# Performance work log

Measured on AMD Instinct MI355X. Metric: run time of the kernel, lower is better.

Reference implementation:

```python
import jax, jax.numpy as jnp
import numpy as np

B, S, D, H = 2, 2048, 1024, 16
HD = D // H  # 64


def setup_inputs() -> dict:
    key = jax.random.key(0)
    ks = jax.random.split(key, 10)
    inp = {
        "queries": jax.random.normal(ks[0], (B, S, D), dtype=jnp.float32),
        "keys": jax.random.normal(ks[1], (B, S, D), dtype=jnp.float32),
        "values": jax.random.normal(ks[2], (B, S, D), dtype=jnp.float32),
        "attention_mask": jax.random.randint(ks[3], (B, S), 0, 2, dtype=jnp.int32),
        # Linear params (torch nn.Linear: y = x @ W.T + b), scaled like default init
        "Wq": jax.random.normal(ks[4], (D, D), dtype=jnp.float32) / np.sqrt(D),
        "bq": jnp.zeros((D,), dtype=jnp.float32),
        "Wk": jax.random.normal(ks[5], (D, D), dtype=jnp.float32) / np.sqrt(D),
        "bk": jnp.zeros((D,), dtype=jnp.float32),
        "Wv": jax.random.normal(ks[6], (D, D), dtype=jnp.float32) / np.sqrt(D),
        "bv": jnp.zeros((D,), dtype=jnp.float32),
    }
    return inp


def _split_heads(x):
    # torch.chunk along last dim + stack(dim=1) == reshape + transpose
    b, s, d = x.shape
    return x.reshape(b, s, H, HD).transpose(0, 2, 1, 3)  # [B,H,S,hd]


def reference(queries, keys, values, attention_mask, Wq, bq, Wk, bk, Wv, bv):
    q = jax.nn.relu(queries @ Wq.T + bq)
    k = jax.nn.relu(keys @ Wk.T + bk)
    v = jax.nn.relu(values @ Wv.T + bv)
    qh, kh, vh = _split_heads(q), _split_heads(k), _split_heads(v)
    score = jnp.einsum("bhqd,bhkd->bhqk", qh, kh) / jnp.sqrt(jnp.float32(HD))
    # enc mask: [B,1,S,1] broadcast over key dim — masks whole query rows where mask==0
    row_mask = (attention_mask == 0)[:, None, :, None]
    score = jnp.where(row_mask, jnp.float32(-1e9), score)
    attn = jax.nn.softmax(score, axis=-1)
    a = jnp.einsum("bhqk,bhkd->bhqd", attn, vh)  # [B,H,S,hd]
    # faithful to original: permute(0,1,3,2) then reshape to (B,S,D)
    a = a.transpose(0, 1, 3, 2).reshape(q.shape[0], q.shape[1], q.shape[2])
    return a + queries
```

## Files before the change

kernel.cpp:

```cpp
#include <hip/hip_runtime.h>
#include <hip/hip_bf16.h>

#define DEV __device__ __forceinline__

typedef __attribute__((ext_vector_type(8))) short short8;
typedef __attribute__((ext_vector_type(4))) float f32x4;

#define MFMA16(a, b, c) __builtin_amdgcn_mfma_f32_16x16x32_bf16((a), (b), (c), 0, 0, 0)

static constexpr int B_ = 2, S_ = 2048, D_ = 1024, H_ = 16, HD_ = 64;
static constexpr long NX = (long)B_ * S_ * D_;
static constexpr long NW = (long)D_ * D_;

DEV short f2bf(float f) {
    __hip_bfloat16 h = __float2bfloat16(f);
    union { __hip_bfloat16 hh; short s; } u;
    u.hh = h;
    return u.s;
}

DEV float bf2f(short s) {
    union { float f; unsigned u; } x;
    x.u = ((unsigned)(unsigned short)s) << 16;
    return x.f;
}

DEV unsigned cvtpk(float a, float b) {
    unsigned r;
    asm("v_cvt_pk_bf16_f32 %0, %1, %2" : "=v"(r) : "v"(a), "v"(b));
    return r;
}

DEV short8 ld8(const short* p) { return *(const short8*)p; }

DEV void gld16(const short* g, short* l) {
    __builtin_amdgcn_global_load_lds(
        (const __attribute__((address_space(1))) unsigned int*)g,
        (__attribute__((address_space(3))) unsigned int*)l, 16, 0, 0);
}

__global__ __launch_bounds__(256) void convert_all(
    const float* __restrict__ q, const float* __restrict__ k, const float* __restrict__ v,
    const float* __restrict__ wq, const float* __restrict__ wk, const float* __restrict__ wv,
    short* __restrict__ qb, short* __restrict__ kb, short* __restrict__ vb,
    short* __restrict__ wqb, short* __restrict__ wkb, short* __restrict__ wvb) {
    long tid = (long)blockIdx.x * 256 + threadIdx.x;
    long e = tid * 4;
    const float* src; short* dst; long off;
    if      (e < NX)            { src = q;  dst = qb;  off = e; }
    else if (e < 2*NX)          { src = k;  dst = kb;  off = e - NX; }
    else if (e < 3*NX)          { src = v;  dst = vb;  off = e - 2*NX; }
    else if (e < 3*NX + NW)     { src = wq; dst = wqb; off = e - 3*NX; }
    else if (e < 3*NX + 2*NW)   { src = wk; dst = wkb; off = e - 3*NX - NW; }
    else                        { src = wv; dst = wvb; off = e - 3*NX - 2*NW; }
    float4 f = *(const float4*)(src + off);
    short4 o;
    o.x = f2bf(f.x); o.y = f2bf(f.y); o.z = f2bf(f.z); o.w = f2bf(f.w);
    *(short4*)(dst + off) = o;
}

__global__ __launch_bounds__(256) void gemm_bias_relu(
    const short* __restrict__ X0, const short* __restrict__ X1, const short* __restrict__ X2,
    const short* __restrict__ W0, const short* __restrict__ W1, const short* __restrict__ W2,
    const float* __restrict__ b0, const float* __restrict__ b1, const float* __restrict__ b2,
    short* __restrict__ O0, short* __restrict__ O1, short* __restrict__ O2) {
    __shared__ short As[2][128 * 32];
    __shared__ short Bs[2][128 * 32];

    const int bid = blockIdx.x;
    const int tl  = (bid & 7) * 96 + (bid >> 3);
    const int bx  = tl & 7;
    const int by  = (tl >> 3) & 31;
    const int z   = tl >> 8;

    const short* X   = (z == 0) ? X0 : (z == 1) ? X1 : X2;
    const short* W   = (z == 0) ? W0 : (z == 1) ? W1 : W2;
    const float* bia = (z == 0) ? b0 : (z == 1) ? b1 : b2;
    short*       Out = (z == 0) ? O0 : (z == 1) ? O1 : O2;

    const int tid  = threadIdx.x;
    const int wid  = tid >> 6;
    const int lane = tid & 63;
    const int id   = lane & 15;
    const int quad = lane >> 4;
    const int m0 = by * 128;
    const int n0 = bx * 128;
    const int wm = (wid >> 1) * 64;
    const int wn = (wid & 1) * 64;

    const short* Ag0 = X + (long)(m0 + wid * 32 + (lane >> 2)) * D_ + (lane & 3) * 8;
    const short* Bg0 = W + (long)(n0 + wid * 32 + (lane >> 2)) * D_ + (lane & 3) * 8;
    const int offW = wid * 1024;

    f32x4 acc[4][4] = {};

    gld16(Ag0,            &As[0][offW]);
    gld16(Ag0 + 16 * D_,  &As[0][offW + 512]);
    gld16(Bg0,            &Bs[0][offW]);
    gld16(Bg0 + 16 * D_,  &Bs[0][offW + 512]);

    for (int kk = 0; kk < D_; kk += 32) {
        const int cur = (kk >> 5) & 1;
        __syncthreads();
        if (kk + 32 < D_) {
            const int nxt = cur ^ 1;
            gld16(Ag0 + kk + 32,            &As[nxt][offW]);
            gld16(Ag0 + 16 * D_ + kk + 32,  &As[nxt][offW + 512]);
            gld16(Bg0 + kk + 32,            &Bs[nxt][offW]);
            gld16(Bg0 + 16 * D_ + kk + 32,  &Bs[nxt][offW + 512]);
        }

        short8 af[4], bf[4];
#pragma unroll
        for (int i = 0; i < 4; i++) af[i] = ld8(&As[cur][(wm + 16*i + id) * 32 + quad * 8]);
#pragma unroll
        for (int j = 0; j < 4; j++) bf[j] = ld8(&Bs[cur][(wn + 16*j + id) * 32 + quad * 8]);
#pragma unroll
        for (int i = 0; i < 4; i++)
#pragma unroll
            for (int j = 0; j < 4; j++)
                acc[i][j] = MFMA16(af[i], bf[j], acc[i][j]);
    }

#pragma unroll
    for (int j = 0; j < 4; j++) {
        int col = n0 + wn + 16*j + id;
        float bj = bia[col];
#pragma unroll
        for (int i = 0; i < 4; i++) {
#pragma unroll
            for (int r = 0; r < 4; r++) {
                int row = m0 + wm + 16*i + quad*4 + r;
                float val = fmaxf(acc[i][j][r] + bj, 0.f);
                Out[(long)row * D_ + col] = f2bf(val);
            }
        }
    }
}

__global__ __launch_bounds__(256) void transpose_v(const short* __restrict__ Vp,
                                                   short* __restrict__ VT) {
    __shared__ short tile[64 * 64];
    const int bh = blockIdx.y;
    const int b = bh >> 4, h = bh & 15;
    const int s0 = blockIdx.x * 64;
    const int t = threadIdx.x;
#pragma unroll
    for (int it = 0; it < 2; it++) {
        int row = (t >> 3) + 32 * it;
        int u   = t & 7;
        short8 d = ld8(Vp + (long)(b * S_ + s0 + row) * D_ + h * HD_ + u * 8);
        *(short8*)(&tile[row * 64 + (u ^ ((row >> 3) & 7)) * 8]) = d;
    }
    __syncthreads();
#pragma unroll
    for (int it = 0; it < 2; it++) {
        int e  = (t >> 3) + 32 * it;
        int sb = (t & 7) * 8;
        short8 o;
#pragma unroll
        for (int u = 0; u < 8; u++) {
            int row = sb + u;
            o[u] = tile[row * 64 + (((e >> 3) ^ ((row >> 3) & 7)) * 8) + (e & 7)];
        }
        *(short8*)(VT + ((long)bh * HD_ + e) * S_ + s0 + sb) = o;
    }
}

__global__ __launch_bounds__(256, 2) void attention(
    const short* __restrict__ Qb, const short* __restrict__ Kb,
    const short* __restrict__ VT, const int* __restrict__ mask,
    const float* __restrict__ queries, float* __restrict__ out) {
    __shared__ short Ks[2][64 * 64];
    __shared__ short Vs[2][64 * 64];
    __shared__ short pl[4][2 * 16 * 72];

    const int tid  = threadIdx.x;
    const int wid  = tid >> 6;
    const int lane = tid & 63;
    const int id   = lane & 15;
    const int quad = lane >> 4;

    const int bid = blockIdx.x;
    const int w   = bid >> 3;
    const int bh  = (bid & 7) + 8 * (w & 3);
    const int qt  = w >> 2;
    const int b   = bh >> 4;
    const int h   = bh & 15;
    const int q0  = qt * 128 + wid * 32;

    short8 qf[2][2];
#pragma unroll
    for (int g = 0; g < 2; g++) {
        const short* qbase = Qb + (long)(b * S_ + q0 + g * 16 + id) * D_ + h * HD_ + quad * 8;
        short8 f0 = ld8(qbase);
        short8 f1 = ld8(qbase + 32);
        const float qsc = mask[b * S_ + q0 + g * 16 + id] ? 0.125f : 0.f;
#pragma unroll
        for (int i = 0; i < 8; i++) {
            f0[i] = f2bf(bf2f(f0[i]) * qsc);
            f1[i] = f2bf(bf2f(f1[i]) * qsc);
        }
        qf[g][0] = f0; qf[g][1] = f1;
    }

    const int srow = wid * 16 + (lane >> 3);
    const int su   = (lane & 7) ^ (srow & 7);
    const short* kg0 = Kb + ((long)b * S_ + srow) * D_ + h * HD_ + su * 8;
    const short* vg0 = VT + (((long)(b * H_ + h) * HD_) + srow) * S_ + su * 8;
    short* plw = pl[wid];

    const int swz = id & 7;

    float l4[2][4] = {};
    f32x4 o[2][4] = {};

    gld16(kg0,            &Ks[0][wid * 1024]);
    gld16(kg0 + 8 * D_,   &Ks[0][wid * 1024 + 512]);
    gld16(vg0,            &Vs[0][wid * 1024]);
    gld16(vg0 + 8 * S_,   &Vs[0][wid * 1024 + 512]);

    for (int c0 = 0; c0 < S_; c0 += 64) {
        const int cur = (c0 >> 6) & 1;
        __syncthreads();
        if (c0 + 64 < S_) {
            const int nxt = cur ^ 1;
            const long cg = (long)(c0 + 64);
            gld16(kg0 + cg * D_,           &Ks[nxt][wid * 1024]);
            gld16(kg0 + cg * D_ + 8 * D_,  &Ks[nxt][wid * 1024 + 512]);
            gld16(vg0 + cg,                &Vs[nxt][wid * 1024]);
            gld16(vg0 + cg + 8 * S_,       &Vs[nxt][wid * 1024 + 512]);
        }

        f32x4 s[2][4];
#pragma unroll
        for (int g = 0; g < 2; g++)
#pragma unroll
            for (int t = 0; t < 4; t++) s[g][t] = (f32x4){0.f, 0.f, 0.f, 0.f};
#pragma unroll
        for (int t = 0; t < 4; t++) {
            short8 a0 = ld8(&Ks[cur][(16*t + id) * 64 + ((quad    ) ^ swz) * 8]);
            short8 a1 = ld8(&Ks[cur][(16*t + id) * 64 + ((quad ^ 4) ^ swz) * 8]);
            s[0][t] = MFMA16(a0, qf[0][0], s[0][t]);
            s[0][t] = MFMA16(a1, qf[0][1], s[0][t]);
            s[1][t] = MFMA16(a0, qf[1][0], s[1][t]);
            s[1][t] = MFMA16(a1, qf[1][1], s[1][t]);
        }

#pragma unroll
        for (int g = 0; g < 2; g++) {
            short* plg = plw + g * (16 * 72);
#pragma unroll
            for (int t = 0; t < 4; t++) {
                float p0 = __expf(s[g][t][0]);
                float p1 = __expf(s[g][t][1]);
                float p2 = __expf(s[g][t][2]);
                float p3 = __expf(s[g][t][3]);
                l4[g][0] += p0; l4[g][1] += p1; l4[g][2] += p2; l4[g][3] += p3;
                uint2 w2;
                w2.x = cvtpk(p0, p1);
                w2.y = cvtpk(p2, p3);
                *(uint2*)(&plg[id * 72 + 16 * t + quad * 4]) = w2;
            }
        }
        short8 pf[2][2];
#pragma unroll
        for (int g = 0; g < 2; g++) {
            short* plg = plw + g * (16 * 72);
            pf[g][0] = ld8(&plg[id * 72 + quad * 8]);
            pf[g][1] = ld8(&plg[id * 72 + 32 + quad * 8]);
        }

#pragma unroll
        for (int j2 = 0; j2 < 4; j2++) {
#pragma unroll
            for (int kh = 0; kh < 2; kh++) {
                short8 va = ld8(&Vs[cur][(16*j2 + id) * 64 + (((kh << 2) + quad) ^ swz) * 8]);
                o[0][j2] = MFMA16(va, pf[0][kh], o[0][j2]);
                o[1][j2] = MFMA16(va, pf[1][kh], o[1][j2]);
            }
        }
    }

    const long obase = (long)b * (S_ * D_) + (long)h * (HD_ * S_);
#pragma unroll
    for (int g = 0; g < 2; g++) {
        float l = l4[g][0] + l4[g][1] + l4[g][2] + l4[g][3];
        l += __shfl_xor(l, 16);
        l += __shfl_xor(l, 32);
        const float linv = 1.f / l;
#pragma unroll
        for (int j2 = 0; j2 < 4; j2++) {
#pragma unroll
            for (int r = 0; r < 4; r++) {
                int dim = 16 * j2 + quad * 4 + r;
                long idx = obase + (long)dim * S_ + q0 + g * 16 + id;
                out[idx] = o[g][j2][r] * linv + queries[idx];
            }
        }
    }
}

extern "C" void kernel_launch(void* const* d_in, const int* in_sizes, int n_in,
                              void* d_out, int out_size, void* d_ws, size_t ws_size,
                              hipStream_t stream) {
    const float* queries = (const float*)d_in[0];
    const float* keys    = (const float*)d_in[1];
    const float* values  = (const float*)d_in[2];
    const int*   mask    = (const int*)d_in[3];
    const float* Wq = (const float*)d_in[4];
    const float* bq = (const float*)d_in[5];
    const float* Wk = (const float*)d_in[6];
    const float* bk = (const float*)d_in[7];
    const float* Wv = (const float*)d_in[8];
    const float* bv = (const float*)d_in[9];
    float* out = (float*)d_out;

    short* ws  = (short*)d_ws;
    short* qb  = ws;
    short* kb  = qb  + NX;
    short* vb  = kb  + NX;
    short* wqb = vb  + NX;
    short* wkb = wqb + NW;
    short* wvb = wkb + NW;
    short* Q   = wvb + NW;
    short* K   = Q   + NX;
    short* Vp  = K   + NX;
    short* VT  = Vp  + NX;

    convert_all<<<15360, 256, 0, stream>>>(queries, keys, values, Wq, Wk, Wv,
                                           qb, kb, vb, wqb, wkb, wvb);
    gemm_bias_relu<<<768, 256, 0, stream>>>(qb, kb, vb, wqb, wkb, wvb,
                                            bq, bk, bv, Q, K, Vp);
    transpose_v<<<dim3(32, 32), 256, 0, stream>>>(Vp, VT);
    attention<<<512, 256, 0, stream>>>(Q, K, VT, mask, queries, out);
}
```

Baseline: 194.0 us.

## Halve query rows per wave in attention to double grid and raise occupancy

Each wave of the attention kernel now handles 16 query rows instead of 32, so a block covers 64 queries and the grid grows from 512 to 1024 blocks. Register and LDS use per block drop, and launch bounds ask for 3 blocks per CU. This is meant to improve occupancy and latency hiding on the 256-CU part. The cost is that every K/V tile is loaded from global memory and LDS twice as often relative to the MFMA work.

Measured after the change: 213.0 us. 1.1x slower.

```diff
diff --git a/kernel.cpp b/kernel.cpp
--- a/kernel.cpp
+++ b/kernel.cpp
@@ -167,13 +167,13 @@
     }
 }
 
-__global__ __launch_bounds__(256, 2) void attention(
+__global__ __launch_bounds__(256, 3) void attention(
     const short* __restrict__ Qb, const short* __restrict__ Kb,
     const short* __restrict__ VT, const int* __restrict__ mask,
     const float* __restrict__ queries, float* __restrict__ out) {
     __shared__ short Ks[2][64 * 64];
     __shared__ short Vs[2][64 * 64];
-    __shared__ short pl[4][2 * 16 * 72];
+    __shared__ short pl[4][16 * 72];
 
     const int tid  = threadIdx.x;
     const int wid  = tid >> 6;
@@ -187,21 +187,20 @@
     const int qt  = w >> 2;
     const int b   = bh >> 4;
     const int h   = bh & 15;
-    const int q0  = qt * 128 + wid * 32;
-
-    short8 qf[2][2];
-#pragma unroll
-    for (int g = 0; g < 2; g++) {
-        const short* qbase = Qb + (long)(b * S_ + q0 + g * 16 + id) * D_ + h * HD_ + quad * 8;
+    const int q0  = qt * 64 + wid * 16;
+
+    short8 qf0, qf1;
+    {
+        const short* qbase = Qb + (long)(b * S_ + q0 + id) * D_ + h * HD_ + quad * 8;
         short8 f0 = ld8(qbase);
         short8 f1 = ld8(qbase + 32);
-        const float qsc = mask[b * S_ + q0 + g * 16 + id] ? 0.125f : 0.f;
+        const float qsc = mask[b * S_ + q0 + id] ? 0.125f : 0.f;
 #pragma unroll
         for (int i = 0; i < 8; i++) {
             f0[i] = f2bf(bf2f(f0[i]) * qsc);
             f1[i] = f2bf(bf2f(f1[i]) * qsc);
         }
-        qf[g][0] = f0; qf[g][1] = f1;
+        qf0 = f0; qf1 = f1;
     }
 
     const int srow = wid * 16 + (lane >> 3);
@@ -212,8 +211,8 @@
 
     const int swz = id & 7;
 
-    float l4[2][4] = {};
-    f32x4 o[2][4] = {};
+    float l4[4] = {};
+    f32x4 o[4] = {};
 
     gld16(kg0,            &Ks[0][wid * 1024]);
     gld16(kg0 + 8 * D_,   &Ks[0][wid * 1024 + 512]);
@@ -232,60 +231,44 @@
             gld16(vg0 + cg + 8 * S_,       &Vs[nxt][wid * 1024 + 512]);
         }
 
-        f32x4 s[2][4];
-#pragma unroll
-        for (int g = 0; g < 2; g++)
-#pragma unroll
-            for (int t = 0; t < 4; t++) s[g][t] = (f32x4){0.f, 0.f, 0.f, 0.f};
+        f32x4 s[4];
+#pragma unroll
+        for (int t = 0; t < 4; t++) s[t] = (f32x4){0.f, 0.f, 0.f, 0.f};
 #pragma unroll
         for (int t = 0; t < 4; t++) {
             short8 a0 = ld8(&Ks[cur][(16*t + id) * 64 + ((quad    ) ^ swz) * 8]);
             short8 a1 = ld8(&Ks[cur][(16*t + id) * 64 + ((quad ^ 4) ^ swz) * 8]);
-            s[0][t] = MFMA16(a0, qf[0][0], s[0][t]);
-            s[0][t] = MFMA16(a1, qf[0][1], s[0][t]);
-            s[1][t] = MFMA16(a0, qf[1][0], s[1][t]);
-            s[1][t] = MFMA16(a1, qf[1][1], s[1][t]);
-        }
-
-#pragma unroll
-        for (int g = 0; g < 2; g++) {
-            short* plg = plw + g * (16 * 72);
-#pragma unroll
-            for (int t = 0; t < 4; t++) {
-                float p0 = __expf(s[g][t][0]);
-                float p1 = __expf(s[g][t][1]);
-                float p2 = __expf(s[g][t][2]);
-                float p3 = __expf(s[g][t][3]);
-                l4[g][0] += p0; l4[g][1] += p1; l4[g][2] += p2; l4[g][3] += p3;
-                uint2 w2;
-                w2.x = cvtpk(p0, p1);
-                w2.y = cvtpk(p2, p3);
-                *(uint2*)(&plg[id * 72 + 16 * t + quad * 4]) = w2;
-            }
-        }
-        short8 pf[2][2];
-#pragma unroll
-        for (int g = 0; g < 2; g++) {
-            short* plg = plw + g * (16 * 72);
-            pf[g][0] = ld8(&plg[id * 72 + quad * 8]);
-            pf[g][1] = ld8(&plg[id * 72 + 32 + quad * 8]);
-        }
+            s[t] = MFMA16(a0, qf0, s[t]);
+            s[t] = MFMA16(a1, qf1, s[t]);
+        }
+
+#pragma unroll
+        for (int t = 0; t < 4; t++) {
+            float p0 = __expf(s[t][0]);
+            float p1 = __expf(s[t][1]);
+            float p2 = __expf(s[t][2]);
+            float p3 = __expf(s[t][3]);
+            l4[0] += p0; l4[1] += p1; l4[2] += p2; l4[3] += p3;
+            uint2 w2;
+            w2.x = cvtpk(p0, p1);
+            w2.y = cvtpk(p2, p3);
+            *(uint2*)(&plw[id * 72 + 16 * t + quad * 4]) = w2;
+        }
+        short8 pf0 = ld8(&plw[id * 72 + quad * 8]);
+        short8 pf1 = ld8(&plw[id * 72 + 32 + quad * 8]);
 
 #pragma unroll
         for (int j2 = 0; j2 < 4; j2++) {
-#pragma unroll
-            for (int kh = 0; kh < 2; kh++) {
-                short8 va = ld8(&Vs[cur][(16*j2 + id) * 64 + (((kh << 2) + quad) ^ swz) * 8]);
-                o[0][j2] = MFMA16(va, pf[0][kh], o[0][j2]);
-                o[1][j2] = MFMA16(va, pf[1][kh], o[1][j2]);
-            }
+            short8 va0 = ld8(&Vs[cur][(16*j2 + id) * 64 + ((quad    ) ^ swz) * 8]);
+            short8 va1 = ld8(&Vs[cur][(16*j2 + id) * 64 + ((quad ^ 4) ^ swz) * 8]);
+            o[j2] = MFMA16(va0, pf0, o[j2]);
+            o[j2] = MFMA16(va1, pf1, o[j2]);
         }
     }
 
     const long obase = (long)b * (S_ * D_) + (long)h * (HD_ * S_);
-#pragma unroll
-    for (int g = 0; g < 2; g++) {
-        float l = l4[g][0] + l4[g][1] + l4[g][2] + l4[g][3];
+    {
+        float l = l4[0] + l4[1] + l4[2] + l4[3];
         l += __shfl_xor(l, 16);
         l += __shfl_xor(l, 32);
         const float linv = 1.f / l;
@@ -294,8 +277,8 @@
 #pragma unroll
             for (int r = 0; r < 4; r++) {
                 int dim = 16 * j2 + quad * 4 + r;
-                long idx = obase + (long)dim * S_ + q0 + g * 16 + id;
-                out[idx] = o[g][j2][r] * linv + queries[idx];
+                long idx = obase + (long)dim * S_ + q0 + id;
+                out[idx] = o[j2][r] * linv + queries[idx];
             }
         }
     }
@@ -333,5 +316,5 @@
     gemm_bias_relu<<<768, 256, 0, stream>>>(qb, kb, vb, wqb, wkb, wvb,
                                             bq, bk, bv, Q, K, Vp);
     transpose_v<<<dim3(32, 32), 256, 0, stream>>>(Vp, VT);
-    attention<<<512, 256, 0, stream>>>(Q, K, VT, mask, queries, out);
-}
+    attention<<<1024, 256, 0, stream>>>(Q, K, VT, mask, queries, out);
+}
```

## Fuse fp32-to-bf16 activation conversion into projection GEMM loads

Applied to the files above, without the earlier changes.

Removes the separate conversion pass over the three activation tensors. The GEMM now loads fp32 activations straight into registers, packs them to bf16, and writes them to LDS after the MFMAs so the loads overlap compute. Only the weights are still converted by a standalone kernel. In exchange, the GEMM reads twice as many A bytes, uses register-staged stores instead of direct-to-LDS loads, and needs more registers.

Measured after the change: 238.8 us. 1.23x slower.

```diff
diff --git a/kernel.cpp b/kernel.cpp
--- a/kernel.cpp
+++ b/kernel.cpp
@@ -31,6 +31,15 @@
     return r;
 }
 
+DEV short8 pk8(float4 lo, float4 hi) {
+    union { short8 s8; unsigned u[4]; } u;
+    u.u[0] = cvtpk(lo.x, lo.y);
+    u.u[1] = cvtpk(lo.z, lo.w);
+    u.u[2] = cvtpk(hi.x, hi.y);
+    u.u[3] = cvtpk(hi.z, hi.w);
+    return u.s8;
+}
+
 DEV short8 ld8(const short* p) { return *(const short8*)p; }
 
 DEV void gld16(const short* g, short* l) {
@@ -39,20 +48,15 @@
         (__attribute__((address_space(3))) unsigned int*)l, 16, 0, 0);
 }
 
-__global__ __launch_bounds__(256) void convert_all(
-    const float* __restrict__ q, const float* __restrict__ k, const float* __restrict__ v,
+__global__ __launch_bounds__(256) void convert_w(
     const float* __restrict__ wq, const float* __restrict__ wk, const float* __restrict__ wv,
-    short* __restrict__ qb, short* __restrict__ kb, short* __restrict__ vb,
     short* __restrict__ wqb, short* __restrict__ wkb, short* __restrict__ wvb) {
     long tid = (long)blockIdx.x * 256 + threadIdx.x;
     long e = tid * 4;
     const float* src; short* dst; long off;
-    if      (e < NX)            { src = q;  dst = qb;  off = e; }
-    else if (e < 2*NX)          { src = k;  dst = kb;  off = e - NX; }
-    else if (e < 3*NX)          { src = v;  dst = vb;  off = e - 2*NX; }
-    else if (e < 3*NX + NW)     { src = wq; dst = wqb; off = e - 3*NX; }
-    else if (e < 3*NX + 2*NW)   { src = wk; dst = wkb; off = e - 3*NX - NW; }
-    else                        { src = wv; dst = wvb; off = e - 3*NX - 2*NW; }
+    if      (e < NW)     { src = wq; dst = wqb; off = e; }
+    else if (e < 2*NW)   { src = wk; dst = wkb; off = e - NW; }
+    else                 { src = wv; dst = wvb; off = e - 2*NW; }
     float4 f = *(const float4*)(src + off);
     short4 o;
     o.x = f2bf(f.x); o.y = f2bf(f.y); o.z = f2bf(f.z); o.w = f2bf(f.w);
@@ -60,7 +64,7 @@
 }
 
 __global__ __launch_bounds__(256) void gemm_bias_relu(
-    const short* __restrict__ X0, const short* __restrict__ X1, const short* __restrict__ X2,
+    const float* __restrict__ X0, const float* __restrict__ X1, const float* __restrict__ X2,
     const short* __restrict__ W0, const short* __restrict__ W1, const short* __restrict__ W2,
     const float* __restrict__ b0, const float* __restrict__ b1, const float* __restrict__ b2,
     short* __restrict__ O0, short* __restrict__ O1, short* __restrict__ O2) {
@@ -73,7 +77,7 @@
     const int by  = (tl >> 3) & 31;
     const int z   = tl >> 8;
 
-    const short* X   = (z == 0) ? X0 : (z == 1) ? X1 : X2;
+    const float* X   = (z == 0) ? X0 : (z == 1) ? X1 : X2;
     const short* W   = (z == 0) ? W0 : (z == 1) ? W1 : W2;
     const float* bia = (z == 0) ? b0 : (z == 1) ? b1 : b2;
     short*       Out = (z == 0) ? O0 : (z == 1) ? O1 : O2;
@@ -88,24 +92,35 @@
     const int wm = (wid >> 1) * 64;
     const int wn = (wid & 1) * 64;
 
-    const short* Ag0 = X + (long)(m0 + wid * 32 + (lane >> 2)) * D_ + (lane & 3) * 8;
+    const float* Ag = X + (long)(m0 + wid * 32 + (lane >> 2)) * D_ + (lane & 3) * 8;
     const short* Bg0 = W + (long)(n0 + wid * 32 + (lane >> 2)) * D_ + (lane & 3) * 8;
     const int offW = wid * 1024;
+    const int aDst = offW + lane * 8;
 
     f32x4 acc[4][4] = {};
 
-    gld16(Ag0,            &As[0][offW]);
-    gld16(Ag0 + 16 * D_,  &As[0][offW + 512]);
-    gld16(Bg0,            &Bs[0][offW]);
-    gld16(Bg0 + 16 * D_,  &Bs[0][offW + 512]);
+    {
+        float4 l0 = *(const float4*)(Ag);
+        float4 h0 = *(const float4*)(Ag + 4);
+        float4 l1 = *(const float4*)(Ag + 16 * D_);
+        float4 h1 = *(const float4*)(Ag + 16 * D_ + 4);
+        gld16(Bg0,            &Bs[0][offW]);
+        gld16(Bg0 + 16 * D_,  &Bs[0][offW + 512]);
+        *(short8*)(&As[0][aDst])       = pk8(l0, h0);
+        *(short8*)(&As[0][aDst + 512]) = pk8(l1, h1);
+    }
 
     for (int kk = 0; kk < D_; kk += 32) {
         const int cur = (kk >> 5) & 1;
+        const int nxt = cur ^ 1;
+        const bool pre = (kk + 32 < D_);
+        float4 l0, h0, l1, h1;
         __syncthreads();
-        if (kk + 32 < D_) {
-            const int nxt = cur ^ 1;
-            gld16(Ag0 + kk + 32,            &As[nxt][offW]);
-            gld16(Ag0 + 16 * D_ + kk + 32,  &As[nxt][offW + 512]);
+        if (pre) {
+            l0 = *(const float4*)(Ag + kk + 32);
+            h0 = *(const float4*)(Ag + kk + 36);
+            l1 = *(const float4*)(Ag + 16 * D_ + kk + 32);
+            h1 = *(const float4*)(Ag + 16 * D_ + kk + 36);
             gld16(Bg0 + kk + 32,            &Bs[nxt][offW]);
             gld16(Bg0 + 16 * D_ + kk + 32,  &Bs[nxt][offW + 512]);
         }
@@ -120,6 +135,11 @@
 #pragma unroll
             for (int j = 0; j < 4; j++)
                 acc[i][j] = MFMA16(af[i], bf[j], acc[i][j]);
+
+        if (pre) {
+            *(short8*)(&As[nxt][aDst])       = pk8(l0, h0);
+            *(short8*)(&As[nxt][aDst + 512]) = pk8(l1, h1);
+        }
     }
 
 #pragma unroll
@@ -317,10 +337,7 @@
     float* out = (float*)d_out;
 
     short* ws  = (short*)d_ws;
-    short* qb  = ws;
-    short* kb  = qb  + NX;
-    short* vb  = kb  + NX;
-    short* wqb = vb  + NX;
+    short* wqb = ws;
     short* wkb = wqb + NW;
     short* wvb = wkb + NW;
     short* Q   = wvb + NW;
@@ -328,9 +345,8 @@
     short* Vp  = K   + NX;
     short* VT  = Vp  + NX;
 
-    convert_all<<<15360, 256, 0, stream>>>(queries, keys, values, Wq, Wk, Wv,
-                                           qb, kb, vb, wqb, wkb, wvb);
-    gemm_bias_relu<<<768, 256, 0, stream>>>(qb, kb, vb, wqb, wkb, wvb,
+    convert_w<<<3072, 256, 0, stream>>>(Wq, Wk, Wv, wqb, wkb, wvb);
+    gemm_bias_relu<<<768, 256, 0, stream>>>(queries, keys, values, wqb, wkb, wvb,
                                             bq, bk, bv, Q, K, Vp);
     transpose_v<<<dim3(32, 32), 256, 0, stream>>>(Vp, VT);
     attention<<<512, 256, 0, stream>>>(Q, K, VT, mask, queries, out);
```
